# Kernel tuning notes

Measured on AMD Instinct MI355X. Metric: run time of the kernel, lower is better.

## Reference

```python
import jax, jax.numpy as jnp
import numpy as np

B, S, H = 4, 4096, 2048
NH = 16
HD = H // NH  # 128


def setup_inputs() -> dict:
    key = jax.random.key(0)
    ks = jax.random.split(key, 11)
    scale = 1.0 / np.sqrt(H)
    inp = {"hidden_states": jax.random.normal(ks[0], (B, S, H), dtype=jnp.float32)}
    names = ["q", "k", "v", "g", "o"]
    for i, n in enumerate(names):
        inp[f"W{n}"] = jax.random.uniform(ks[1 + i], (H, H), dtype=jnp.float32, minval=-scale, maxval=scale)
        inp[f"b{n}"] = jax.random.uniform(ks[6 + i], (H,), dtype=jnp.float32, minval=-scale, maxval=scale)
    return inp


def reference(hidden_states, Wq, bq, Wk, bk, Wv, bv, Wg, bg, Wo, bo):
    x = hidden_states
    b, s, _ = x.shape

    def heads(t):  # [b,s,H] -> [b,nh,s,hd]
        return t.reshape(b, s, NH, HD).transpose(0, 2, 1, 3)

    q = heads(x @ Wq + bq)
    k = heads(x @ Wk + bk)
    v = heads(x @ Wv + bv)
    g = heads(jax.nn.sigmoid(x @ Wg + bg))
    # kv state: [b,h,d,e]; small per-head outer-product sum over seq
    kv = jnp.einsum('bhsd,bhse->bhde', k, v)
    out = jnp.einsum('bhsd,bhde->bhse', q, kv)
    out = (out * g).transpose(0, 2, 1, 3).reshape(b, s, -1)
    return out @ Wo + bo
```

## Files before the change

kernel.cpp:

```cpp
#include <hip/hip_runtime.h>
#include <stdint.h>

typedef unsigned short u16;
typedef unsigned int   u32;
typedef __bf16 bf16x8 __attribute__((ext_vector_type(8)));
typedef float  f32x4  __attribute__((ext_vector_type(4)));
typedef u16    u16x8  __attribute__((ext_vector_type(8)));
typedef u16    u16x4  __attribute__((ext_vector_type(4)));

#define NB    4
#define NS    4096
#define NHID  2048
#define NHEAD 16
#define HDIM  128
#define NKT   32

__device__ __forceinline__ u16 f2bf(float f) {
  u32 u = __builtin_bit_cast(u32, f);
  u = (u + 0x7fffu + ((u >> 16) & 1u)) >> 16;
  return (u16)u;
}
__device__ __forceinline__ float bf2f(u16 h) {
  return __builtin_bit_cast(float, ((u32)h) << 16);
}

__device__ __forceinline__ void async_copy16(u16* lds_dst, const u16* g_src) {
  __builtin_amdgcn_global_load_lds(
      (__attribute__((address_space(1))) u32*)(const_cast<u16*>(g_src)),
      (__attribute__((address_space(3))) u32*)(lds_dst),
      16, 0, 0);
}

#define SBAR()  __builtin_amdgcn_sched_barrier(0)
#define BARRIER() do { SBAR(); __builtin_amdgcn_s_barrier(); SBAR(); } while (0)
#define LGKM0() asm volatile("s_waitcnt lgkmcnt(0)" ::: "memory")
#define VM0()   asm volatile("s_waitcnt vmcnt(0)"   ::: "memory")

__device__ __forceinline__ void stage9(u16* dst, const u16* src, int kt, int tid)
{
#pragma unroll
  for (int i = 0; i < 2; ++i) {
    const int U = (i << 9) + tid;
    const int r = U >> 3, u = U & 7;
    const int col = (kt << 6) + ((u ^ (r & 7)) << 3);
    async_copy16(dst + U * 8, src + (size_t)r * 2048 + col);
  }
}

__device__ __forceinline__ void rd_a(bf16x8 (&d)[4], const u16* base,
                                     int kg, int mq, int lg, int lr)
{
#pragma unroll
  for (int m = 0; m < 4; ++m) {
    const int row = (mq << 6) + (m << 4) + lr;
    const int c = ((kg << 2) | lg) ^ (row & 7);
    d[m] = *(const bf16x8*)(base + row * 64 + (c << 3));
  }
}

__device__ __forceinline__ void rd_b(bf16x8 (&d)[4], const u16* base,
                                     int kg, int lg, int lr)
{
#pragma unroll
  for (int n = 0; n < 4; ++n) {
    const int row = (n << 4) + lr;
    const int c = ((kg << 2) | lg) ^ (row & 7);
    d[n] = *(const bf16x8*)(base + row * 64 + (c << 3));
  }
}

template<bool SWAP>
__device__ __forceinline__ void mmcl(f32x4 (&acc)[8][4], int mq,
                                     const bf16x8 (&a)[4], const bf16x8 (&b)[4])
{
  __builtin_amdgcn_s_setprio(1);
#pragma unroll
  for (int mm = 0; mm < 4; ++mm)
#pragma unroll
    for (int n = 0; n < 4; ++n) {
      if (SWAP)
        acc[mq * 4 + mm][n] = __builtin_amdgcn_mfma_f32_16x16x32_bf16(b[n], a[mm], acc[mq * 4 + mm][n], 0, 0, 0);
      else
        acc[mq * 4 + mm][n] = __builtin_amdgcn_mfma_f32_16x16x32_bf16(a[mm], b[n], acc[mq * 4 + mm][n], 0, 0, 0);
    }
  __builtin_amdgcn_s_setprio(0);
}

template<bool SWAP>
__device__ __forceinline__ void gemm9(const u16* __restrict__ A,
                                      const u16* __restrict__ B,
                                      f32x4 (&acc)[8][4], u16* L)
{
  const int tid = threadIdx.x, lane = tid & 63, w = tid >> 6;
  const int wr = w >> 2, wc = w & 3, lg = lane >> 4, lr = lane & 15;

#pragma unroll
  for (int m = 0; m < 8; ++m)
#pragma unroll
    for (int n = 0; n < 4; ++n) acc[m][n] = f32x4{0.f, 0.f, 0.f, 0.f};

  const u16* A1 = A + (size_t)128 * 2048;
  const u16* B1 = B + (size_t)128 * 2048;
  const int aoff = wr * 8192;
  const int boff = 16384 + ((wc >> 1) * 8192) + ((wc & 1) * 4096);

  stage9(L,                 A,  0, tid);
  stage9(L + 8192,          A1, 0, tid);
  stage9(L + 16384,         B,  0, tid);
  stage9(L + 16384 + 8192,  B1, 0, tid);
  VM0();
  BARRIER();

  bf16x8 aRa[4], aRb[4], bR0[4], bR1[4];
  rd_a(aRa, L + aoff, 0, 0, lg, lr);
  rd_b(bR0, L + boff, 0, lg, lr);
  LGKM0();

#pragma unroll 1
  for (int t = 0; t < NKT - 1; ++t) {
    u16* Lc = L + ((t & 1) << 15);
    u16* Ln = L + (((t + 1) & 1) << 15);
    stage9(Ln,                A,  t + 1, tid);
    stage9(Ln + 16384,        B,  t + 1, tid);
    BARRIER();
    rd_a(aRb, Lc + aoff, 0, 1, lg, lr);
    mmcl<SWAP>(acc, 0, aRa, bR0);
    LGKM0();
    stage9(Ln + 8192,         A1, t + 1, tid);
    stage9(Ln + 16384 + 8192, B1, t + 1, tid);
    BARRIER();
    rd_a(aRa, Lc + aoff, 1, 0, lg, lr);
    rd_b(bR1, Lc + boff, 1, lg, lr);
    mmcl<SWAP>(acc, 1, aRb, bR0);
    LGKM0();
    BARRIER();
    rd_a(aRb, Lc + aoff, 1, 1, lg, lr);
    mmcl<SWAP>(acc, 0, aRa, bR1);
    LGKM0();
    VM0();
    BARRIER();
    rd_a(aRa, Ln + aoff, 0, 0, lg, lr);
    rd_b(bR0, Ln + boff, 0, lg, lr);
    mmcl<SWAP>(acc, 1, aRb, bR1);
    LGKM0();
  }
  {
    u16* Lc = L + (((NKT - 1) & 1) << 15);
    BARRIER();
    rd_a(aRb, Lc + aoff, 0, 1, lg, lr);
    mmcl<SWAP>(acc, 0, aRa, bR0);
    LGKM0();
    BARRIER();
    rd_a(aRa, Lc + aoff, 1, 0, lg, lr);
    rd_b(bR1, Lc + boff, 1, lg, lr);
    mmcl<SWAP>(acc, 1, aRb, bR0);
    LGKM0();
    BARRIER();
    rd_a(aRb, Lc + aoff, 1, 1, lg, lr);
    mmcl<SWAP>(acc, 0, aRa, bR1);
    LGKM0();
    BARRIER();
    mmcl<SWAP>(acc, 1, aRb, bR1);
  }
}

__global__ __launch_bounds__(512, 2) void k_gemm_qkvg(
    const u16* __restrict__ xb, const u16* __restrict__ WT,
    const float* __restrict__ bias,
    u16* __restrict__ q, u16* __restrict__ kT, u16* __restrict__ vT,
    u16* __restrict__ g)
{
  __shared__ u16 L[65536];
  const int bid = blockIdx.x;
  const int grp = bid >> 8, r = bid & 255;
  const int mt = ((grp & 3) << 4) + (r & 15);
  const int nt = ((grp >> 2) << 4) + (r >> 4);
  const size_t bm0 = (size_t)mt << 8;
  const int    bn0 = nt << 8;
  const int nblk = bn0 >> 11;
  const int ocol0 = bn0 & 2047;

  const int tid = threadIdx.x, lane = tid & 63, w = tid >> 6;
  const int wr = w >> 2, wc = w & 3, lg = lane >> 4, lr = lane & 15;

  f32x4 acc[8][4];
  const u16* Ap = xb + bm0 * NHID;
  const u16* Bp = WT + (size_t)bn0 * NHID;

  if (nblk == 0 || nblk == 3) {
    gemm9<true>(Ap, Bp, acc, L);
    u16* outp = (nblk == 0) ? q : g;
    const bool sig = (nblk == 3);
#pragma unroll
    for (int m = 0; m < 8; ++m) {
      const size_t row = bm0 + (wr << 7) + (m << 4) + lr;
#pragma unroll
      for (int n = 0; n < 4; ++n) {
        const int colb = (wc << 6) + (n << 4) + (lg << 2);
        const float* bp = bias + bn0 + colb;
        u16x4 o;
#pragma unroll
        for (int j = 0; j < 4; ++j) {
          float val = acc[m][n][j] + bp[j];
          if (sig) val = 1.f / (1.f + __expf(-val));
          o[j] = f2bf(val);
        }
        *(u16x4*)(outp + row * NHID + ocol0 + colb) = o;
      }
    }
  } else {
    gemm9<false>(Ap, Bp, acc, L);
    u16* outp = (nblk == 1) ? kT : vT;
    const int b = (int)(bm0 >> 12);
    const int srow0 = (int)(bm0 & 4095) + (wr << 7) + (lg << 2);
#pragma unroll
    for (int m = 0; m < 8; ++m) {
      const int srow = srow0 + (m << 4);
#pragma unroll
      for (int n = 0; n < 4; ++n) {
        const int cg = ocol0 + (wc << 6) + (n << 4) + lr;
        const int h = cg >> 7, d = cg & 127;
        const float bia = bias[bn0 + (wc << 6) + (n << 4) + lr];
        u16x4 o;
#pragma unroll
        for (int j = 0; j < 4; ++j) o[j] = f2bf(acc[m][n][j] + bia);
        *(u16x4*)(outp + (((size_t)(b * NHEAD + h) * HDIM + d) << 12) + srow) = o;
      }
    }
  }
}

__global__ __launch_bounds__(512, 2) void k_gemm_out(
    const u16* __restrict__ attn, const u16* __restrict__ WoT,
    const float* __restrict__ bo, float* __restrict__ out)
{
  __shared__ u16 L[65536];
  const int bid = blockIdx.x;
  const int grp = bid >> 7, rr = bid & 127;
  const int mt = (grp << 4) + (rr & 15);
  const int nt = rr >> 4;
  const size_t bm0 = (size_t)mt << 8;
  const int    bn0 = nt << 8;

  const int tid = threadIdx.x, lane = tid & 63, w = tid >> 6;
  const int wr = w >> 2, wc = w & 3, lg = lane >> 4, lr = lane & 15;

  f32x4 acc[8][4];
  gemm9<true>(attn + bm0 * NHID, WoT + (size_t)bn0 * NHID, acc, L);

#pragma unroll
  for (int m = 0; m < 8; ++m) {
    const size_t row = bm0 + (wr << 7) + (m << 4) + lr;
#pragma unroll
    for (int n = 0; n < 4; ++n) {
      const int colb = bn0 + (wc << 6) + (n << 4) + (lg << 2);
      f32x4 o;
#pragma unroll
      for (int j = 0; j < 4; ++j) o[j] = acc[m][n][j] + bo[colb + j];
      *(f32x4*)(out + row * NHID + colb) = o;
    }
  }
}

__device__ __forceinline__ void gemm_core(const u16* A, int lda,
                                          const u16* B, int ldb,
                                          int K, f32x4 acc[4][4],
                                          u16* As, u16* Bs)
{
  const int tid  = threadIdx.x;
  const int lane = tid & 63;
  const int w    = tid >> 6;
  const int wr   = (w >> 1) << 6;
  const int wc   = (w & 1) << 6;
  const int lg   = lane >> 4;
  const int lr   = lane & 15;

#pragma unroll
  for (int m = 0; m < 4; ++m)
#pragma unroll
    for (int n = 0; n < 4; ++n) acc[m][n] = f32x4{0.f, 0.f, 0.f, 0.f};

  for (int k0 = 0; k0 < K; k0 += 32) {
#pragma unroll
    for (int issue = 0; issue < 2; ++issue) {
      int c   = issue * 256 + tid;
      int row = c >> 2, cc = (c & 3) << 3;
      async_copy16(As + c * 8, A + (size_t)row * lda + k0 + cc);
    }
#pragma unroll
    for (int issue = 0; issue < 2; ++issue) {
      int c   = issue * 256 + tid;
      int row = c >> 2, cc = (c & 3) << 3;
      async_copy16(Bs + c * 8, B + (size_t)row * ldb + k0 + cc);
    }
    __syncthreads();

    bf16x8 af[4], bv[4];
#pragma unroll
    for (int m = 0; m < 4; ++m)
      af[m] = *(const bf16x8*)(As + ((wr + m * 16 + lr) << 5) + (lg << 3));
#pragma unroll
    for (int n = 0; n < 4; ++n)
      bv[n] = *(const bf16x8*)(Bs + ((wc + n * 16 + lr) << 5) + (lg << 3));

#pragma unroll
    for (int m = 0; m < 4; ++m)
#pragma unroll
      for (int n = 0; n < 4; ++n)
        acc[m][n] = __builtin_amdgcn_mfma_f32_16x16x32_bf16(af[m], bv[n], acc[m][n], 0, 0, 0);

    __syncthreads();
  }
}

__global__ __launch_bounds__(256) void k_gemm_kv(
    const u16* __restrict__ vT, const u16* __restrict__ kT, float* __restrict__ part)
{
  __shared__ u16 As[128 * 32];
  __shared__ u16 Bs[128 * 32];
  const int bh = blockIdx.x, sp = blockIdx.y;
  const u16* A  = vT + (size_t)bh * (HDIM * NS) + sp * 512;
  const u16* Bt = kT + (size_t)bh * (HDIM * NS) + sp * 512;
  f32x4 acc[4][4];
  gemm_core(A, NS, Bt, NS, 512, acc, As, Bs);

  float* outp = part + ((size_t)sp * 64 + bh) * 16384;
  const int tid = threadIdx.x, lane = tid & 63, w = tid >> 6;
  const int wr = (w >> 1) << 6, wc = (w & 1) << 6, lg = lane >> 4, lr = lane & 15;
#pragma unroll
  for (int m = 0; m < 4; ++m)
#pragma unroll
    for (int n = 0; n < 4; ++n) {
      const int col = wc + n * 16 + lr;
#pragma unroll
      for (int j = 0; j < 4; ++j) {
        const int row = wr + m * 16 + lg * 4 + j;
        outp[row * 128 + col] = acc[m][n][j];
      }
    }
}

__global__ __launch_bounds__(256) void k_gemm_attn(
    const u16* __restrict__ q, const u16* __restrict__ kvT,
    const u16* __restrict__ g, u16* __restrict__ attn)
{
  __shared__ u16 As[128 * 32];
  __shared__ u16 Bs[128 * 32];
  const int st = blockIdx.x, bh = blockIdx.y;
  const int b = bh >> 4, h = bh & 15;
  const size_t bs0 = (size_t)b * NS + st * 128;
  f32x4 acc[4][4];
  gemm_core(q + bs0 * NHID + h * HDIM, NHID, kvT + (size_t)bh * 16384, HDIM, HDIM, acc, As, Bs);

  const int tid = threadIdx.x, lane = tid & 63, w = tid >> 6;
  const int wr = (w >> 1) << 6, wc = (w & 1) << 6, lg = lane >> 4, lr = lane & 15;
#pragma unroll
  for (int m = 0; m < 4; ++m)
#pragma unroll
    for (int n = 0; n < 4; ++n) {
      const int col = wc + n * 16 + lr;
#pragma unroll
      for (int j = 0; j < 4; ++j) {
        const int row = wr + m * 16 + lg * 4 + j;
        const size_t idx = (bs0 + row) * NHID + h * HDIM + col;
        attn[idx] = f2bf(acc[m][n][j] * bf2f(g[idx]));
      }
    }
}

__global__ __launch_bounds__(256) void k_cvt_x(const float* __restrict__ x, u16* __restrict__ xb)
{
  const size_t i = (size_t)blockIdx.x * 256 + threadIdx.x;
  const float4* xf = (const float4*)x;
  float4 a = xf[2 * i];
  float4 b = xf[2 * i + 1];
  u16x8 o;
  o[0] = f2bf(a.x); o[1] = f2bf(a.y); o[2] = f2bf(a.z); o[3] = f2bf(a.w);
  o[4] = f2bf(b.x); o[5] = f2bf(b.y); o[6] = f2bf(b.z); o[7] = f2bf(b.w);
  ((u16x8*)xb)[i] = o;
}

__global__ __launch_bounds__(256) void k_cvt_w_t(const float* __restrict__ W, u16* __restrict__ WT)
{
  __shared__ u16 t[64][72];
  const int kt = blockIdx.x, nt = blockIdx.y;
  const int tid = threadIdx.x;
#pragma unroll
  for (int pass = 0; pass < 4; ++pass) {
    int c = pass * 256 + tid;
    int r = c >> 4, cc = (c & 15) << 2;
    float4 vv = *(const float4*)(W + (size_t)(kt * 64 + r) * 2048 + nt * 64 + cc);
    u16x4 o;
    o[0] = f2bf(vv.x); o[1] = f2bf(vv.y); o[2] = f2bf(vv.z); o[3] = f2bf(vv.w);
    *(u16x4*)&t[r][cc] = o;
  }
  __syncthreads();
#pragma unroll
  for (int pass = 0; pass < 2; ++pass) {
    int c = pass * 256 + tid;
    int rn = c >> 3, cs = (c & 7) << 3;
    u16x8 o;
#pragma unroll
    for (int j = 0; j < 8; ++j) o[j] = t[cs + j][rn];
    *(u16x8*)(WT + (size_t)(nt * 64 + rn) * 2048 + kt * 64 + cs) = o;
  }
}

__global__ __launch_bounds__(256) void k_bias_cat(
    const float* __restrict__ bq, const float* __restrict__ bk,
    const float* __restrict__ bv, const float* __restrict__ bg, float* __restrict__ o)
{
  const int i = blockIdx.x * 256 + threadIdx.x;
  const int blk = i >> 11;
  const float* s = (blk == 0) ? bq : (blk == 1) ? bk : (blk == 2) ? bv : bg;
  o[i] = s[i & 2047];
}

__global__ __launch_bounds__(256) void k_kv_reduce(const float* __restrict__ part, u16* __restrict__ kvT)
{
  const int i = blockIdx.x * 256 + threadIdx.x;
  float s = 0.f;
#pragma unroll
  for (int sp = 0; sp < 8; ++sp) s += part[(size_t)sp * 1048576 + i];
  kvT[i] = f2bf(s);
}

extern "C" void kernel_launch(void* const* d_in, const int* in_sizes, int n_in,
                              void* d_out, int out_size, void* d_ws, size_t ws_size,
                              hipStream_t stream)
{
  const float* x  = (const float*)d_in[0];
  const float* Wq = (const float*)d_in[1];
  const float* bq = (const float*)d_in[2];
  const float* Wk = (const float*)d_in[3];
  const float* bk = (const float*)d_in[4];
  const float* Wv = (const float*)d_in[5];
  const float* bv = (const float*)d_in[6];
  const float* Wg = (const float*)d_in[7];
  const float* bg = (const float*)d_in[8];
  const float* Wo = (const float*)d_in[9];
  const float* bo = (const float*)d_in[10];
  float* out = (float*)d_out;

  char* ws = (char*)d_ws;
  u16*   xb   = (u16*)(ws + 0x00000000ULL);
  u16*   WT   = (u16*)(ws + 0x04000000ULL);
  u16*   WoT  = (u16*)(ws + 0x06000000ULL);
  float* bias = (float*)(ws + 0x06800000ULL);
  u16*   q    = (u16*)(ws + 0x06900000ULL);
  u16*   kT   = (u16*)(ws + 0x0A900000ULL);
  u16*   vT   = (u16*)(ws + 0x0E900000ULL);
  u16*   gg   = (u16*)(ws + 0x12900000ULL);
  u16*   kvT  = (u16*)(ws + 0x16900000ULL);
  float* part = (float*)WT;
  u16*   attn = xb;

  if (ws_size < 0x16B00000ULL) return;

  k_cvt_x<<<16384, 256, 0, stream>>>(x, xb);
  k_cvt_w_t<<<dim3(32, 32), 256, 0, stream>>>(Wq, WT);
  k_cvt_w_t<<<dim3(32, 32), 256, 0, stream>>>(Wk, WT + (size_t)2048 * 2048);
  k_cvt_w_t<<<dim3(32, 32), 256, 0, stream>>>(Wv, WT + (size_t)2 * 2048 * 2048);
  k_cvt_w_t<<<dim3(32, 32), 256, 0, stream>>>(Wg, WT + (size_t)3 * 2048 * 2048);
  k_cvt_w_t<<<dim3(32, 32), 256, 0, stream>>>(Wo, WoT);
  k_bias_cat<<<32, 256, 0, stream>>>(bq, bk, bv, bg, bias);

  k_gemm_qkvg<<<2048, 512, 0, stream>>>(xb, WT, bias, q, kT, vT, gg);

  k_gemm_kv<<<dim3(64, 8), 256, 0, stream>>>(vT, kT, part);
  k_kv_reduce<<<4096, 256, 0, stream>>>(part, kvT);

  k_gemm_attn<<<dim3(32, 64), 256, 0, stream>>>(q, kvT, gg, attn);
  k_gemm_out<<<512, 512, 0, stream>>>(attn, WoT, bo, out);
}
```

Baseline: 794.3 us.

## Split LDS tiles by k-half with new swizzle and partial vmcnt waits

Changes the LDS staging layout so that each 256x64 k-tile is stored as two 32-column halves, with a 4-way XOR swizzle on 64-byte rows. Fragment reads become simple constant-offset loads. Full vmcnt(0) waits are replaced by vmcnt(4), so the second half of the next tile's loads can stay in flight while the first half is consumed. This is meant to cut LDS address arithmetic and shorten stalls in the double-buffered GEMM loop, at the cost of relying on exact in-order accounting of outstanding loads for correctness.

Result: slower. 878.6 us (+10.6%).

```diff
diff --git a/kernel.cpp b/kernel.cpp
--- a/kernel.cpp
+++ b/kernel.cpp
@@ -35,38 +35,32 @@
 #define BARRIER() do { SBAR(); __builtin_amdgcn_s_barrier(); SBAR(); } while (0)
 #define LGKM0() asm volatile("s_waitcnt lgkmcnt(0)" ::: "memory")
 #define VM0()   asm volatile("s_waitcnt vmcnt(0)"   ::: "memory")
-
-__device__ __forceinline__ void stage9(u16* dst, const u16* src, int kt, int tid)
+#define VM4()   asm volatile("s_waitcnt vmcnt(4)"   ::: "memory")
+
+__device__ __forceinline__ void stage10(u16* dst, const u16* src,
+                                        int kt, int kg, int tid)
 {
 #pragma unroll
   for (int i = 0; i < 2; ++i) {
     const int U = (i << 9) + tid;
-    const int r = U >> 3, u = U & 7;
-    const int col = (kt << 6) + ((u ^ (r & 7)) << 3);
+    const int r = U >> 2, u = U & 3;
+    const int col = (kt << 6) + (kg << 5) + ((u ^ ((r >> 1) & 3)) << 3);
     async_copy16(dst + U * 8, src + (size_t)r * 2048 + col);
   }
 }
 
-__device__ __forceinline__ void rd_a(bf16x8 (&d)[4], const u16* base,
-                                     int kg, int mq, int lg, int lr)
-{
-#pragma unroll
-  for (int m = 0; m < 4; ++m) {
-    const int row = (mq << 6) + (m << 4) + lr;
-    const int c = ((kg << 2) | lg) ^ (row & 7);
-    d[m] = *(const bf16x8*)(base + row * 64 + (c << 3));
-  }
-}
-
-__device__ __forceinline__ void rd_b(bf16x8 (&d)[4], const u16* base,
-                                     int kg, int lg, int lr)
-{
-#pragma unroll
-  for (int n = 0; n < 4; ++n) {
-    const int row = (n << 4) + lr;
-    const int c = ((kg << 2) | lg) ^ (row & 7);
-    d[n] = *(const bf16x8*)(base + row * 64 + (c << 3));
-  }
+__device__ __forceinline__ void rdA(bf16x8 (&d)[4], const u16* base, int mq)
+{
+#pragma unroll
+  for (int m = 0; m < 4; ++m)
+    d[m] = *(const bf16x8*)(base + mq * 2048 + m * 512);
+}
+
+__device__ __forceinline__ void rdB(bf16x8 (&d)[4], const u16* base)
+{
+#pragma unroll
+  for (int n = 0; n < 4; ++n)
+    d[n] = *(const bf16x8*)(base + n * 512);
 }
 
 template<bool SWAP>
@@ -87,76 +81,77 @@
 }
 
 template<bool SWAP>
-__device__ __forceinline__ void gemm9(const u16* __restrict__ A,
-                                      const u16* __restrict__ B,
-                                      f32x4 (&acc)[8][4], u16* L)
+__device__ __forceinline__ void gemm10(const u16* __restrict__ A,
+                                       const u16* __restrict__ B,
+                                       f32x4 (&acc)[8][4], u16* L)
 {
   const int tid = threadIdx.x, lane = tid & 63, w = tid >> 6;
   const int wr = w >> 2, wc = w & 3, lg = lane >> 4, lr = lane & 15;
+  const int ggx = ((lg ^ ((lr >> 1) & 3)) << 3);
+  const int arow = wr * 4096 + lr * 32 + ggx;
+  const int brow = wc * 2048 + lr * 32 + ggx;
 
 #pragma unroll
   for (int m = 0; m < 8; ++m)
 #pragma unroll
     for (int n = 0; n < 4; ++n) acc[m][n] = f32x4{0.f, 0.f, 0.f, 0.f};
 
-  const u16* A1 = A + (size_t)128 * 2048;
-  const u16* B1 = B + (size_t)128 * 2048;
-  const int aoff = wr * 8192;
-  const int boff = 16384 + ((wc >> 1) * 8192) + ((wc & 1) * 4096);
-
-  stage9(L,                 A,  0, tid);
-  stage9(L + 8192,          A1, 0, tid);
-  stage9(L + 16384,         B,  0, tid);
-  stage9(L + 16384 + 8192,  B1, 0, tid);
+  stage10(L,         A, 0, 0, tid);
+  stage10(L + 16384, B, 0, 0, tid);
+  SBAR();
+  stage10(L + 8192,  A, 0, 1, tid);
+  stage10(L + 24576, B, 0, 1, tid);
   VM0();
   BARRIER();
 
   bf16x8 aRa[4], aRb[4], bR0[4], bR1[4];
-  rd_a(aRa, L + aoff, 0, 0, lg, lr);
-  rd_b(bR0, L + boff, 0, lg, lr);
+  rdA(aRa, L + arow, 0);
+  rdB(bR0, L + 16384 + brow);
   LGKM0();
 
 #pragma unroll 1
   for (int t = 0; t < NKT - 1; ++t) {
     u16* Lc = L + ((t & 1) << 15);
     u16* Ln = L + (((t + 1) & 1) << 15);
-    stage9(Ln,                A,  t + 1, tid);
-    stage9(Ln + 16384,        B,  t + 1, tid);
-    BARRIER();
-    rd_a(aRb, Lc + aoff, 0, 1, lg, lr);
+    stage10(Ln,         A, t + 1, 0, tid);
+    stage10(Ln + 16384, B, t + 1, 0, tid);
+    VM4();
+    BARRIER();
+    rdA(aRb, Lc + arow, 1);
     mmcl<SWAP>(acc, 0, aRa, bR0);
     LGKM0();
-    stage9(Ln + 8192,         A1, t + 1, tid);
-    stage9(Ln + 16384 + 8192, B1, t + 1, tid);
-    BARRIER();
-    rd_a(aRa, Lc + aoff, 1, 0, lg, lr);
-    rd_b(bR1, Lc + boff, 1, lg, lr);
+    stage10(Ln + 8192,  A, t + 1, 1, tid);
+    stage10(Ln + 24576, B, t + 1, 1, tid);
+    BARRIER();
+    rdA(aRa, Lc + 8192 + arow, 0);
+    rdB(bR1, Lc + 24576 + brow);
     mmcl<SWAP>(acc, 1, aRb, bR0);
     LGKM0();
     BARRIER();
-    rd_a(aRb, Lc + aoff, 1, 1, lg, lr);
+    rdA(aRb, Lc + 8192 + arow, 1);
     mmcl<SWAP>(acc, 0, aRa, bR1);
     LGKM0();
-    VM0();
-    BARRIER();
-    rd_a(aRa, Ln + aoff, 0, 0, lg, lr);
-    rd_b(bR0, Ln + boff, 0, lg, lr);
+    VM4();
+    BARRIER();
+    rdA(aRa, Ln + arow, 0);
+    rdB(bR0, Ln + 16384 + brow);
     mmcl<SWAP>(acc, 1, aRb, bR1);
     LGKM0();
   }
   {
     u16* Lc = L + (((NKT - 1) & 1) << 15);
-    BARRIER();
-    rd_a(aRb, Lc + aoff, 0, 1, lg, lr);
+    VM0();
+    BARRIER();
+    rdA(aRb, Lc + arow, 1);
     mmcl<SWAP>(acc, 0, aRa, bR0);
     LGKM0();
     BARRIER();
-    rd_a(aRa, Lc + aoff, 1, 0, lg, lr);
-    rd_b(bR1, Lc + boff, 1, lg, lr);
+    rdA(aRa, Lc + 8192 + arow, 0);
+    rdB(bR1, Lc + 24576 + brow);
     mmcl<SWAP>(acc, 1, aRb, bR0);
     LGKM0();
     BARRIER();
-    rd_a(aRb, Lc + aoff, 1, 1, lg, lr);
+    rdA(aRb, Lc + 8192 + arow, 1);
     mmcl<SWAP>(acc, 0, aRa, bR1);
     LGKM0();
     BARRIER();
@@ -188,7 +183,7 @@
   const u16* Bp = WT + (size_t)bn0 * NHID;
 
   if (nblk == 0 || nblk == 3) {
-    gemm9<true>(Ap, Bp, acc, L);
+    gemm10<true>(Ap, Bp, acc, L);
     u16* outp = (nblk == 0) ? q : g;
     const bool sig = (nblk == 3);
 #pragma unroll
@@ -209,7 +204,7 @@
       }
     }
   } else {
-    gemm9<false>(Ap, Bp, acc, L);
+    gemm10<false>(Ap, Bp, acc, L);
     u16* outp = (nblk == 1) ? kT : vT;
     const int b = (int)(bm0 >> 12);
     const int srow0 = (int)(bm0 & 4095) + (wr << 7) + (lg << 2);
@@ -246,7 +241,7 @@
   const int wr = w >> 2, wc = w & 3, lg = lane >> 4, lr = lane & 15;
 
   f32x4 acc[8][4];
-  gemm9<true>(attn + bm0 * NHID, WoT + (size_t)bn0 * NHID, acc, L);
+  gemm10<true>(attn + bm0 * NHID, WoT + (size_t)bn0 * NHID, acc, L);
 
 #pragma unroll
   for (int m = 0; m < 8; ++m) {
```

## Cut per-k-step barriers in GEMM main loop and merge weight-conversion launches

Applied to the files above, without the earlier changes.

The main GEMM loop is restructured to issue all four next-tile stage loads up front and to keep a single LDS wait, a single VM wait and one barrier per k-step instead of several. The epilogue tail also drops its barriers and waits. This aims to remove synchronisation stalls between MFMA clusters so they run back to back. The five weight transpose/convert launches are merged into one 3D-grid launch to cut launch overhead. Dropping the lgkmcnt waits between LDS reads and MFMA use relies on the compiler inserting the needed waits itself, and staging into the other buffer early depends on the single barrier being enough to prevent write-after-read hazards.

After: 777.1 us (median of 2 runs). 2.2% less time.

```diff
diff --git a/kernel.cpp b/kernel.cpp
--- a/kernel.cpp
+++ b/kernel.cpp
@@ -87,9 +87,9 @@
 }
 
 template<bool SWAP>
-__device__ __forceinline__ void gemm9(const u16* __restrict__ A,
-                                      const u16* __restrict__ B,
-                                      f32x4 (&acc)[8][4], u16* L)
+__device__ __forceinline__ void gemm13(const u16* __restrict__ A,
+                                       const u16* __restrict__ B,
+                                       f32x4 (&acc)[8][4], u16* L)
 {
   const int tid = threadIdx.x, lane = tid & 63, w = tid >> 6;
   const int wr = w >> 2, wc = w & 3, lg = lane >> 4, lr = lane & 15;
@@ -114,52 +114,38 @@
   bf16x8 aRa[4], aRb[4], bR0[4], bR1[4];
   rd_a(aRa, L + aoff, 0, 0, lg, lr);
   rd_b(bR0, L + boff, 0, lg, lr);
-  LGKM0();
 
 #pragma unroll 1
   for (int t = 0; t < NKT - 1; ++t) {
-    u16* Lc = L + ((t & 1) << 15);
+    const u16* Lc = L + ((t & 1) << 15);
     u16* Ln = L + (((t + 1) & 1) << 15);
     stage9(Ln,                A,  t + 1, tid);
+    stage9(Ln + 8192,         A1, t + 1, tid);
     stage9(Ln + 16384,        B,  t + 1, tid);
-    BARRIER();
+    stage9(Ln + 16384 + 8192, B1, t + 1, tid);
     rd_a(aRb, Lc + aoff, 0, 1, lg, lr);
     mmcl<SWAP>(acc, 0, aRa, bR0);
-    LGKM0();
-    stage9(Ln + 8192,         A1, t + 1, tid);
-    stage9(Ln + 16384 + 8192, B1, t + 1, tid);
-    BARRIER();
     rd_a(aRa, Lc + aoff, 1, 0, lg, lr);
     rd_b(bR1, Lc + boff, 1, lg, lr);
     mmcl<SWAP>(acc, 1, aRb, bR0);
-    LGKM0();
-    BARRIER();
     rd_a(aRb, Lc + aoff, 1, 1, lg, lr);
     mmcl<SWAP>(acc, 0, aRa, bR1);
+    mmcl<SWAP>(acc, 1, aRb, bR1);
     LGKM0();
     VM0();
     BARRIER();
     rd_a(aRa, Ln + aoff, 0, 0, lg, lr);
     rd_b(bR0, Ln + boff, 0, lg, lr);
-    mmcl<SWAP>(acc, 1, aRb, bR1);
-    LGKM0();
   }
   {
-    u16* Lc = L + (((NKT - 1) & 1) << 15);
-    BARRIER();
+    const u16* Lc = L + (((NKT - 1) & 1) << 15);
     rd_a(aRb, Lc + aoff, 0, 1, lg, lr);
     mmcl<SWAP>(acc, 0, aRa, bR0);
-    LGKM0();
-    BARRIER();
     rd_a(aRa, Lc + aoff, 1, 0, lg, lr);
     rd_b(bR1, Lc + boff, 1, lg, lr);
     mmcl<SWAP>(acc, 1, aRb, bR0);
-    LGKM0();
-    BARRIER();
     rd_a(aRb, Lc + aoff, 1, 1, lg, lr);
     mmcl<SWAP>(acc, 0, aRa, bR1);
-    LGKM0();
-    BARRIER();
     mmcl<SWAP>(acc, 1, aRb, bR1);
   }
 }
@@ -188,7 +174,7 @@
   const u16* Bp = WT + (size_t)bn0 * NHID;
 
   if (nblk == 0 || nblk == 3) {
-    gemm9<true>(Ap, Bp, acc, L);
+    gemm13<true>(Ap, Bp, acc, L);
     u16* outp = (nblk == 0) ? q : g;
     const bool sig = (nblk == 3);
 #pragma unroll
@@ -209,7 +195,7 @@
       }
     }
   } else {
-    gemm9<false>(Ap, Bp, acc, L);
+    gemm13<false>(Ap, Bp, acc, L);
     u16* outp = (nblk == 1) ? kT : vT;
     const int b = (int)(bm0 >> 12);
     const int srow0 = (int)(bm0 & 4095) + (wr << 7) + (lg << 2);
@@ -246,7 +232,7 @@
   const int wr = w >> 2, wc = w & 3, lg = lane >> 4, lr = lane & 15;
 
   f32x4 acc[8][4];
-  gemm9<true>(attn + bm0 * NHID, WoT + (size_t)bn0 * NHID, acc, L);
+  gemm13<true>(attn + bm0 * NHID, WoT + (size_t)bn0 * NHID, acc, L);
 
 #pragma unroll
   for (int m = 0; m < 8; ++m) {
@@ -380,10 +366,17 @@
   ((u16x8*)xb)[i] = o;
 }
 
-__global__ __launch_bounds__(256) void k_cvt_w_t(const float* __restrict__ W, u16* __restrict__ WT)
+__global__ __launch_bounds__(256) void k_cvt_w_t5(
+    const float* __restrict__ Wq, const float* __restrict__ Wk,
+    const float* __restrict__ Wv, const float* __restrict__ Wg,
+    const float* __restrict__ Wo,
+    u16* __restrict__ WT, u16* __restrict__ WoT)
 {
   __shared__ u16 t[64][72];
-  const int kt = blockIdx.x, nt = blockIdx.y;
+  const int kt = blockIdx.x, nt = blockIdx.y, z = blockIdx.z;
+  const float* W = (z == 0) ? Wq : (z == 1) ? Wk : (z == 2) ? Wv
+                 : (z == 3) ? Wg : Wo;
+  u16* dst = (z == 4) ? WoT : (WT + (size_t)z * 2048 * 2048);
   const int tid = threadIdx.x;
 #pragma unroll
   for (int pass = 0; pass < 4; ++pass) {
@@ -402,7 +395,7 @@
     u16x8 o;
 #pragma unroll
     for (int j = 0; j < 8; ++j) o[j] = t[cs + j][rn];
-    *(u16x8*)(WT + (size_t)(nt * 64 + rn) * 2048 + kt * 64 + cs) = o;
+    *(u16x8*)(dst + (size_t)(nt * 64 + rn) * 2048 + kt * 64 + cs) = o;
   }
 }
 
@@ -458,11 +451,7 @@
   if (ws_size < 0x16B00000ULL) return;
 
   k_cvt_x<<<16384, 256, 0, stream>>>(x, xb);
-  k_cvt_w_t<<<dim3(32, 32), 256, 0, stream>>>(Wq, WT);
-  k_cvt_w_t<<<dim3(32, 32), 256, 0, stream>>>(Wk, WT + (size_t)2048 * 2048);
-  k_cvt_w_t<<<dim3(32, 32), 256, 0, stream>>>(Wv, WT + (size_t)2 * 2048 * 2048);
-  k_cvt_w_t<<<dim3(32, 32), 256, 0, stream>>>(Wg, WT + (size_t)3 * 2048 * 2048);
-  k_cvt_w_t<<<dim3(32, 32), 256, 0, stream>>>(Wo, WoT);
+  k_cvt_w_t5<<<dim3(32, 32, 5), 256, 0, stream>>>(Wq, Wk, Wv, Wg, Wo, WT, WoT);
   k_bias_cat<<<32, 256, 0, stream>>>(bq, bk, bv, bg, bias);
 
   k_gemm_qkvg<<<2048, 512, 0, stream>>>(xb, WT, bias, q, kT, vT, gg);
```
